# Kernel optimization log

Measured on AMD Instinct MI355X. Metric: run time of the kernel, lower is better.

## Reference

```python
import jax, jax.numpy as jnp
import numpy as np

N = 200000
B = 2
BEV_SIZES = [(376, 376), (188, 188), (94, 94), (188, 188), (94, 94)]
VOXELS = [40000, 20000, 10000, 20000, 10000]
IN_SCALES = 3
D_PT = 9        # point_feature_dim
D_AVFE = 64
D_AVFEO = 128
FINFO_MIN = float(np.finfo(np.float32).min)  # torch fills scatter_max output with finfo.min


def _make_vfs(V, H, W):
    # unique (batch, y, x) voxel coordinates for the dense scatter_nd
    total = B * H * W
    flat = np.arange(V, dtype=np.int64) * (total // V)
    b = flat // (H * W)
    r = flat % (H * W)
    return jnp.asarray(np.stack([b, r // W, r % W], axis=1), dtype=jnp.int32)


def setup_inputs():
    key = jax.random.key(0)
    ks = jax.random.split(key, 16)
    inp = {"points": jax.random.normal(ks[0], (N, 4), jnp.float32)}
    for i in range(5):
        inp[f"vlc{i}"] = jax.random.uniform(ks[1 + i], (N, 3), jnp.float32)
        inp[f"pv{i}"] = jax.random.randint(ks[6 + i], (N,), 0, VOXELS[i], dtype=jnp.int32)
        inp[f"vfs{i}"] = _make_vfs(VOXELS[i], *BEV_SIZES[i])
    s = 0.05
    inp["W_avfe_point"] = jax.random.normal(ks[11], (D_PT, D_AVFE), jnp.float32) * s
    inp["W_avfe_att"] = jax.random.normal(ks[12], (2 * D_PT, D_AVFE), jnp.float32) * s
    inp["W_avfeo_point"] = jax.random.normal(ks[13], (IN_SCALES * 2 * D_AVFE, D_AVFEO), jnp.float32) * s
    inp["W_avfeo_att"] = jax.random.normal(ks[14], (2 * D_PT, D_AVFEO), jnp.float32) * s
    inp["batch_size"] = B
    return inp


def _seg_mean_gather(x, idx, V):
    # scatterMean: per-voxel mean gathered back to points -> [N, C]
    s = jax.ops.segment_sum(x, idx, num_segments=V)
    cnt = jax.ops.segment_sum(jnp.ones((x.shape[0], 1), x.dtype), idx, num_segments=V)
    return (s / jnp.maximum(cnt, 1.0))[idx]


def _seg_max(x, idx, V):
    # scatterMax with torch finfo.min init for empty voxels
    return jnp.maximum(jax.ops.segment_max(x, idx, num_segments=V), FINFO_MIN)


def _scale_inputs(points, vlc, pv, V):
    pm = _seg_mean_gather(points, pv, V)                      # [N,4]
    plc = points[:, :3] - pm[:, :3]                            # [N,3]
    pif = jnp.concatenate([points, plc, vlc[:, :2]], axis=1)   # [N,9]
    a2 = _seg_mean_gather(pif, pv, V)                          # [N,9]
    a1 = jnp.concatenate([plc, pif[:, 3:]], axis=1)            # [N,9]
    att = jnp.concatenate([a1, a2], axis=1)                    # [N,18]
    return pif, att


def _dense(vfs, feat, batch_size, H, W):
    # scatter_nd into [B,H,W,C] then channels-first
    out = jnp.zeros((batch_size, H, W, feat.shape[1]), feat.dtype)
    out = out.at[vfs[:, 0], vfs[:, 1], vfs[:, 2]].set(feat)
    return jnp.transpose(out, (0, 3, 1, 2))


def reference(points, vlc0, vlc1, vlc2, vlc3, vlc4,
              W_avfe_point, W_avfe_att, W_avfeo_point, W_avfeo_att,
              pv0, pv1, pv2, pv3, pv4,
              vfs0, vfs1, vfs2, vfs3, vfs4, batch_size):
    vlcs = [vlc0, vlc1, vlc2, vlc3, vlc4]
    pvs = [pv0, pv1, pv2, pv3, pv4]
    vfss = [vfs0, vfs1, vfs2, vfs3, vfs4]

    avfe = []
    for i in range(IN_SCALES):
        V = vfss[i].shape[0]
        pif, att = _scale_inputs(points, vlcs[i], pvs[i], V)
        pfc = pif @ W_avfe_point                 # [N,64]
        afc = att @ W_avfe_att                   # [N,64]
        final = afc * pfc
        vf = _seg_max(final, pvs[i], V)          # [V,64]
        avfe.append(jnp.concatenate([final, vf[pvs[i]]], axis=1))  # [N,128]

    feat = jnp.concatenate(avfe, axis=1)         # [N,384]
    pfc_o = feat @ W_avfeo_point                 # [N,128]

    outs = []
    for i in range(IN_SCALES, len(vfss)):
        V = vfss[i].shape[0]
        pif, att = _scale_inputs(points, vlcs[i], pvs[i], V)
        afc = att @ W_avfeo_att                  # [N,128]
        final = afc * pfc_o
        vf = _seg_max(final, pvs[i], V)          # [V,128]
        H, W = BEV_SIZES[i]
        outs.append(_dense(vfss[i], vf, batch_size, H, W))
    return tuple(outs)
```

## Files before the change

### kernel.cpp

```cpp
#include <hip/hip_runtime.h>
#include <stdint.h>

#define N_PTS 200000
#define HW3 35344
#define HW4 8836
#define OUT4_OFF 9048064
#define OUT_ELEMS 11310080
#define S_FLOATS 1000000
#define F_UINTS  2240000
#define G_USHORTS 3840000
#define G4_OFF 2560000
typedef unsigned short ushort_t;

__device__ __forceinline__ float bfbits2f(unsigned hbits16) {
  return __uint_as_float(hbits16 << 16);
}
__device__ __forceinline__ ushort_t f2bf(float f) {
  if (!(f == f)) return (ushort_t)0;
  unsigned u = __float_as_uint(f);
  if ((u & 0x7F800000u) == 0x7F800000u)
    return (ushort_t)(((u >> 16) & 0x8000u) | 0x7F7Fu);
  unsigned r = u + 0x7FFFu + ((u >> 16) & 1u);
  ushort_t h = (ushort_t)(r >> 16);
  if ((h & 0x7FFFu) == 0x7F80u) h = (ushort_t)((h & 0x8000u) | 0x7F7Fu);
  return h;
}
__device__ __forceinline__ unsigned enc16(unsigned h) {
  return (h & 0x8000u) ? (h ^ 0xFFFFu) : (h | 0x8000u);
}
__device__ __forceinline__ unsigned dec16(unsigned e) {
  return (e & 0x8000u) ? (e & 0x7FFFu) : (e ^ 0xFFFFu);
}

__device__ __forceinline__ float decSafeF(unsigned e) {
  unsigned d = dec16(e & 0xFFFFu);
  if ((d & 0x7F80u) == 0x7F80u) d = 0;
  return bfbits2f(d);
}

__device__ __forceinline__ void casMax16(ushort_t* o16, size_t pos, unsigned enc) {
  unsigned* w = (unsigned*)(o16 + (pos & ~(size_t)1));
  unsigned sh = ((unsigned)pos & 1u) << 4;
  unsigned old = *w;
  while (true) {
    unsigned cur = (old >> sh) & 0xFFFFu;
    if (enc <= cur) break;
    unsigned nw = (old & ~(0xFFFFu << sh)) | (enc << sh);
    unsigned prev = atomicCAS(w, old, nw);
    if (prev == old) break;
    old = prev;
  }
}
__device__ __forceinline__ void casMaxPair(unsigned* w, unsigned lo, unsigned hi) {
  unsigned old = *w;
  while (true) {
    unsigned clo = old & 0xFFFFu, chi = old >> 16;
    unsigned nlo = lo > clo ? lo : clo;
    unsigned nhi = hi > chi ? hi : chi;
    unsigned nw = nlo | (nhi << 16);
    if (nw == old) break;
    unsigned prev = atomicCAS(w, old, nw);
    if (prev == old) break;
    old = prev;
  }
}

struct ScaleArgs {
  const ushort_t* vlc[5];
  const int*      pv[5];
  float*          stats[5];
  unsigned*       vf16[3];
};

__global__ void k_init(unsigned* __restrict__ outw, unsigned* __restrict__ g) {
  int i = blockIdx.x * blockDim.x + threadIdx.x;
  if (i < S_FLOATS) { outw[i] = 0u; return; }
  if (i < S_FLOATS + F_UINTS) { outw[i] = 0x00800080u; return; }
  i -= S_FLOATS + F_UINTS;
  if (i < G_USHORTS / 2) g[i] = 0x00800080u;
}

__global__ void __launch_bounds__(256) k_segsum(const ushort4* __restrict__ points, ScaleArgs a) {
  int p = blockIdx.x * blockDim.x + threadIdx.x;
  if (p >= N_PTS) return;
  ushort4 pu = points[p];
  float px = bfbits2f(pu.x), py = bfbits2f(pu.y), pz = bfbits2f(pu.z), pw = bfbits2f(pu.w);
  #pragma unroll
  for (int s = 0; s < 5; s++) {
    int v = a.pv[s][p];
    float l0 = bfbits2f(a.vlc[s][3 * p + 0]);
    float l1 = bfbits2f(a.vlc[s][3 * p + 1]);
    float* st = a.stats[s] + (size_t)v * 10;
    atomicAdd(st + 0, px);
    atomicAdd(st + 1, py);
    atomicAdd(st + 2, pz);
    atomicAdd(st + 3, pw);
    atomicAdd(st + 4, l0);
    atomicAdd(st + 5, l1);
    atomicAdd(st + 9, 1.0f);
  }
}

__global__ void k_voxstats(ScaleArgs a) {
  int i = blockIdx.x * blockDim.x + threadIdx.x;
  int s, v;
  if      (i <  40000) { s = 0; v = i; }
  else if (i <  60000) { s = 1; v = i - 40000; }
  else if (i <  70000) { s = 2; v = i - 60000; }
  else if (i <  90000) { s = 3; v = i - 70000; }
  else if (i < 100000) { s = 4; v = i - 90000; }
  else return;
  float* st = a.stats[s] + (size_t)v * 10;
  float cnt = st[9];
  float c = fmaxf(cnt, 1.0f);
  float s0 = st[0], s1 = st[1], s2 = st[2], s3 = st[3], s4 = st[4], s5 = st[5];
  float pm0 = s0 / c, pm1 = s1 / c, pm2 = s2 / c, pm3 = s3 / c;
  float mp0 = (s0 - cnt * pm0) / c;
  float mp1 = (s1 - cnt * pm1) / c;
  float mp2 = (s2 - cnt * pm2) / c;
  float mv0 = s4 / c, mv1 = s5 / c;
  st[0] = pm0; st[1] = pm1; st[2] = pm2; st[3] = pm3;
  st[4] = mp0; st[5] = mp1; st[6] = mp2; st[7] = mv0; st[8] = mv1;
}

__global__ void __launch_bounds__(256) k_scale012(
    const ushort4* __restrict__ points, ScaleArgs a,
    const ushort_t* __restrict__ Wp,
    const ushort_t* __restrict__ Wa) {
  __shared__ float WpS[9 * 64];
  __shared__ float WaS[18 * 64];
  int tid = threadIdx.x;
  for (int i = tid; i < 9 * 64; i += 256)  WpS[i] = bfbits2f(Wp[i]);
  for (int i = tid; i < 18 * 64; i += 256) WaS[i] = bfbits2f(Wa[i]);
  __syncthreads();

  int p = blockIdx.x * blockDim.x + tid;
  if (p >= N_PTS) return;
  ushort4 pu = points[p];
  float px = bfbits2f(pu.x), py = bfbits2f(pu.y), pz = bfbits2f(pu.z), pw = bfbits2f(pu.w);
  #pragma unroll 1
  for (int s = 0; s < 3; s++) {
    int v = a.pv[s][p];
    const float* st = a.stats[s] + (size_t)v * 10;
    float a2[9];
    #pragma unroll
    for (int k = 0; k < 9; k++) a2[k] = st[k];
    float plc0 = px - a2[0], plc1 = py - a2[1], plc2 = pz - a2[2];
    float vl0 = bfbits2f(a.vlc[s][3 * p + 0]);
    float vl1 = bfbits2f(a.vlc[s][3 * p + 1]);
    float pif[9] = {px, py, pz, pw, plc0, plc1, plc2, vl0, vl1};
    float att[18] = {plc0, plc1, plc2, pw, plc0, plc1, plc2, vl0, vl1,
                     a2[0], a2[1], a2[2], a2[3], a2[4], a2[5], a2[6], a2[7], a2[8]};
    unsigned* vfw = a.vf16[s] + (size_t)v * 32;
    #pragma unroll 1
    for (int cb = 0; cb < 64; cb += 16) {
      float accp[16], acca[16];
      #pragma unroll
      for (int l = 0; l < 16; l++) { accp[l] = 0.0f; acca[l] = 0.0f; }
      #pragma unroll
      for (int k = 0; k < 9; k++) {
        float x = pif[k];
        #pragma unroll
        for (int l = 0; l < 16; l++) accp[l] = fmaf(x, WpS[k * 64 + cb + l], accp[l]);
      }
      #pragma unroll
      for (int k = 0; k < 18; k++) {
        float x = att[k];
        #pragma unroll
        for (int l = 0; l < 16; l++) acca[l] = fmaf(x, WaS[k * 64 + cb + l], acca[l]);
      }
      #pragma unroll
      for (int l = 0; l < 16; l += 2) {
        unsigned lo = enc16(f2bf(acca[l] * accp[l]));
        unsigned hi = enc16(f2bf(acca[l + 1] * accp[l + 1]));
        casMaxPair(vfw + ((cb + l) >> 1), lo, hi);
      }
    }
  }
}

struct K4Args {
  const ushort4* points;
  const ushort_t* vlc[5];
  const int* pv[5];
  const float* stats[5];
  const unsigned* vf16[3];
  ushort_t* G;
  const ushort_t* Wp;
  const ushort_t* Wa;
  const ushort_t* Wpo;
  const ushort_t* Wao;
};

__global__ void __launch_bounds__(256, 2) k_big(K4Args a) {
  __shared__ __align__(16) float A[64][68];
  __shared__ __align__(16) unsigned Bw16[64][64];
  __shared__ __align__(16) float WaoS[18][128];
  __shared__ __align__(16) float WpS[9][64];
  __shared__ __align__(16) float WaS[18][64];
  __shared__ __align__(16) float attS[64][20];
  __shared__ int pvAll[5][64];

  int tid = threadIdx.x;
  int p0 = blockIdx.x * 64;

  for (int i = tid; i < 18 * 128; i += 256) WaoS[0][i] = bfbits2f(a.Wao[i]);
  for (int i = tid; i < 9 * 64; i += 256)   WpS[0][i]  = bfbits2f(a.Wp[i]);
  for (int i = tid; i < 18 * 64; i += 256)  WaS[0][i]  = bfbits2f(a.Wa[i]);
  if (tid < 64) {
    #pragma unroll
    for (int s = 0; s < 5; s++) pvAll[s][tid] = a.pv[s][p0 + tid];
  }
  float4 pt = make_float4(0.f, 0.f, 0.f, 0.f);
  if (tid < 64) {
    ushort4 pu = a.points[p0 + tid];
    pt = make_float4(bfbits2f(pu.x), bfbits2f(pu.y), bfbits2f(pu.z), bfbits2f(pu.w));
  }
  __syncthreads();

  int pr = tid & 7;
  int cg = tid >> 3;
  int cb4 = cg << 2;
  int cb2 = cg << 1;

  float acc[8][4];
  #pragma unroll
  for (int j = 0; j < 8; j++)
    #pragma unroll
    for (int l = 0; l < 4; l++) acc[j][l] = 0.0f;

  #pragma unroll 1
  for (int kc = 0; kc < 6; kc++) {
    {
      const uint4* src = (const uint4*)(a.Wpo + (size_t)kc * 64 * 128);
      uint4* dst = (uint4*)&Bw16[0][0];
      for (int i = tid; i < 1024; i += 256) dst[i] = src[i];
    }
    int s = kc >> 1;
    if ((kc & 1) == 0) {
      if (tid < 64) {
        int v = pvAll[s][tid];
        const float* st = a.stats[s] + (size_t)v * 10;
        float a2k[9];
        #pragma unroll
        for (int k = 0; k < 9; k++) a2k[k] = st[k];
        float vl0 = bfbits2f(a.vlc[s][3 * (p0 + tid) + 0]);
        float vl1 = bfbits2f(a.vlc[s][3 * (p0 + tid) + 1]);
        float* row = attS[tid];
        row[0] = pt.x; row[1] = pt.y; row[2] = pt.z; row[3] = pt.w;
        row[4] = pt.x - a2k[0]; row[5] = pt.y - a2k[1]; row[6] = pt.z - a2k[2];
        row[7] = vl0; row[8] = vl1;
        #pragma unroll
        for (int k = 0; k < 9; k++) row[9 + k] = a2k[k];
      }
      __syncthreads();
      int p = tid >> 2, ch0 = (tid & 3) << 4;
      float pv_[18];
      #pragma unroll
      for (int k = 0; k < 18; k++) pv_[k] = attS[p][k];
      float accp[16], acca[16];
      #pragma unroll
      for (int l = 0; l < 16; l++) { accp[l] = 0.0f; acca[l] = 0.0f; }
      #pragma unroll
      for (int k = 0; k < 9; k++) {
        float x = pv_[k];
        #pragma unroll
        for (int l = 0; l < 16; l++) accp[l] = fmaf(x, WpS[k][ch0 + l], accp[l]);
      }
      #pragma unroll
      for (int k = 0; k < 18; k++) {
        int src = (k < 3) ? (4 + k) : (k == 3) ? 3 : k;
        float x = pv_[src];
        #pragma unroll
        for (int l = 0; l < 16; l++) acca[l] = fmaf(x, WaS[k][ch0 + l], acca[l]);
      }
      #pragma unroll
      for (int l4 = 0; l4 < 16; l4 += 4) {
        float4 f;
        f.x = accp[l4 + 0] * acca[l4 + 0];
        f.y = accp[l4 + 1] * acca[l4 + 1];
        f.z = accp[l4 + 2] * acca[l4 + 2];
        f.w = accp[l4 + 3] * acca[l4 + 3];
        *(float4*)&A[p][ch0 + l4] = f;
      }
    } else {
      const unsigned* vfw = a.vf16[s];
      for (int i = tid; i < 2048; i += 256) {
        int p = i >> 5; int w = i & 31;
        int v = pvAll[s][p];
        unsigned q = vfw[(size_t)v * 32 + w];
        A[p][2 * w]     = decSafeF(q & 0xFFFFu);
        A[p][2 * w + 1] = decSafeF(q >> 16);
      }
    }
    __syncthreads();
    #pragma unroll 2
    for (int kk = 0; kk < 64; kk += 4) {
      float4 av[8];
      #pragma unroll
      for (int j = 0; j < 8; j++) av[j] = *(const float4*)&A[pr + (j << 3)][kk];
      #pragma unroll
      for (int t = 0; t < 4; t++) {
        unsigned w0 = Bw16[kk + t][cb2], w1 = Bw16[kk + t][cb2 + 1];
        float b0 = __uint_as_float(w0 << 16);
        float b1 = __uint_as_float(w0 & 0xFFFF0000u);
        float b2 = __uint_as_float(w1 << 16);
        float b3 = __uint_as_float(w1 & 0xFFFF0000u);
        #pragma unroll
        for (int j = 0; j < 8; j++) {
          float x = (t == 0) ? av[j].x : (t == 1) ? av[j].y : (t == 2) ? av[j].z : av[j].w;
          acc[j][0] = fmaf(x, b0, acc[j][0]);
          acc[j][1] = fmaf(x, b1, acc[j][1]);
          acc[j][2] = fmaf(x, b2, acc[j][2]);
          acc[j][3] = fmaf(x, b3, acc[j][3]);
        }
      }
    }
    __syncthreads();
  }

  #pragma unroll 1
  for (int si = 0; si < 2; si++) {
    if (tid < 64) {
      int v = pvAll[3 + si][tid];
      const float* st = a.stats[3 + si] + (size_t)v * 10;
      float a2k[9];
      #pragma unroll
      for (int k = 0; k < 9; k++) a2k[k] = st[k];
      float vl0 = bfbits2f(a.vlc[3 + si][3 * (p0 + tid) + 0]);
      float vl1 = bfbits2f(a.vlc[3 + si][3 * (p0 + tid) + 1]);
      float plc0 = pt.x - a2k[0], plc1 = pt.y - a2k[1], plc2 = pt.z - a2k[2];
      float* row = attS[tid];
      row[0] = plc0; row[1] = plc1; row[2] = plc2; row[3] = pt.w;
      row[4] = plc0; row[5] = plc1; row[6] = plc2; row[7] = vl0; row[8] = vl1;
      #pragma unroll
      for (int k = 0; k < 9; k++) row[9 + k] = a2k[k];
    }
    __syncthreads();
    size_t gbase = si ? (size_t)G4_OFF : 0;
    float afc[8][4];
    #pragma unroll
    for (int j = 0; j < 8; j++)
      #pragma unroll
      for (int l = 0; l < 4; l++) afc[j][l] = 0.0f;
    #pragma unroll
    for (int k = 0; k < 18; k++) {
      float4 w = *(const float4*)&WaoS[k][cb4];
      #pragma unroll
      for (int j = 0; j < 8; j++) {
        float x = attS[pr + (j << 3)][k];
        afc[j][0] = fmaf(x, w.x, afc[j][0]);
        afc[j][1] = fmaf(x, w.y, afc[j][1]);
        afc[j][2] = fmaf(x, w.z, afc[j][2]);
        afc[j][3] = fmaf(x, w.w, afc[j][3]);
      }
    }
    #pragma unroll
    for (int j = 0; j < 8; j++) {
      int p = pr + (j << 3);
      int v = pvAll[3 + si][p];
      #pragma unroll
      for (int l = 0; l < 4; l++) {
        float f = afc[j][l] * acc[j][l];
        casMax16(a.G, gbase + (size_t)v * 128 + (cb4 + l), enc16(f2bf(f)));
      }
    }
    __syncthreads();
  }
}

__global__ void k_clear(unsigned* __restrict__ outw) {
  int i = blockIdx.x * blockDim.x + threadIdx.x;
  if (i < OUT_ELEMS / 2) outw[i] = 0u;
}

__global__ void __launch_bounds__(256) k_scatter_out(const ushort_t* __restrict__ G,
                                                     const int* __restrict__ vfs3,
                                                     const int* __restrict__ vfs4,
                                                     ushort_t* __restrict__ out16) {
  int i = blockIdx.x * blockDim.x + threadIdx.x;
  if (i >= G_USHORTS) return;
  int s, idx;
  if (i < G4_OFF) { s = 0; idx = i; }
  else            { s = 1; idx = i - G4_OFF; }
  int v = idx >> 7, c = idx & 127;
  const int* vfs = s ? vfs4 : vfs3;
  int b = vfs[3 * v], y = vfs[3 * v + 1], x = vfs[3 * v + 2];
  size_t pos;
  if (s) pos = (size_t)OUT4_OFF + (((size_t)(b * 128 + c) * 94 + y) * 94 + x);
  else   pos = ((size_t)(b * 128 + c) * 188 + y) * 188 + x;
  unsigned d = dec16(G[i]);
  if ((d & 0x7F80u) == 0x7F80u) d = (d & 0x8000u) | 0x7F7Fu;
  out16[pos] = (ushort_t)d;
}

extern "C" void kernel_launch(void* const* d_in, const int* in_sizes, int n_in,
                              void* d_out, int out_size, void* d_ws, size_t ws_size,
                              hipStream_t stream) {
  static const int VOX[5] = {40000, 20000, 10000, 20000, 10000};

  const ushort_t* points = (const ushort_t*)d_in[0];
  const ushort_t* vlc[5]; const int* pv[5]; const int* vfs[5];
  const ushort_t *Wp, *Wa, *Wpo, *Wao;
  if (in_sizes[2] == N_PTS) {
    for (int s = 0; s < 5; s++) {
      vlc[s] = (const ushort_t*)d_in[1 + 3 * s];
      pv[s]  = (const int*)     d_in[2 + 3 * s];
      vfs[s] = (const int*)     d_in[3 + 3 * s];
    }
    Wp  = (const ushort_t*)d_in[16];
    Wa  = (const ushort_t*)d_in[17];
    Wpo = (const ushort_t*)d_in[18];
    Wao = (const ushort_t*)d_in[19];
  } else {
    for (int s = 0; s < 5; s++) vlc[s] = (const ushort_t*)d_in[1 + s];
    Wp  = (const ushort_t*)d_in[6];
    Wa  = (const ushort_t*)d_in[7];
    Wpo = (const ushort_t*)d_in[8];
    Wao = (const ushort_t*)d_in[9];
    for (int s = 0; s < 5; s++) pv[s]  = (const int*)d_in[10 + s];
    for (int s = 0; s < 5; s++) vfs[s] = (const int*)d_in[15 + s];
  }

  float* statsBase = (float*)d_out;
  unsigned* outw = (unsigned*)d_out;
  unsigned* fBase = outw + S_FLOATS;
  ushort_t* G = (ushort_t*)d_ws;
  ushort_t* out16 = (ushort_t*)d_out;

  float* stats[5];
  size_t offS = 0;
  for (int s = 0; s < 5; s++) { stats[s] = statsBase + offS; offS += (size_t)VOX[s] * 10; }
  unsigned* vf16[3];
  size_t offF = 0;
  for (int s = 0; s < 3; s++) { vf16[s] = fBase + offF; offF += (size_t)VOX[s] * 32; }

  ScaleArgs sa;
  for (int s = 0; s < 5; s++) { sa.vlc[s] = vlc[s]; sa.pv[s] = pv[s]; sa.stats[s] = stats[s]; }
  for (int s = 0; s < 3; s++) sa.vf16[s] = vf16[s];

  int totInit = S_FLOATS + F_UINTS + G_USHORTS / 2;
  k_init<<<(totInit + 255) / 256, 256, 0, stream>>>(outw, (unsigned*)d_ws);

  k_segsum<<<(N_PTS + 255) / 256, 256, 0, stream>>>((const ushort4*)points, sa);

  k_voxstats<<<(100000 + 255) / 256, 256, 0, stream>>>(sa);

  k_scale012<<<(N_PTS + 255) / 256, 256, 0, stream>>>((const ushort4*)points, sa, Wp, Wa);

  K4Args ka;
  ka.points = (const ushort4*)points;
  for (int s = 0; s < 5; s++) { ka.vlc[s] = vlc[s]; ka.pv[s] = pv[s]; ka.stats[s] = stats[s]; }
  for (int s = 0; s < 3; s++) ka.vf16[s] = vf16[s];
  ka.G = G;
  ka.Wp = Wp; ka.Wa = Wa; ka.Wpo = Wpo; ka.Wao = Wao;
  k_big<<<N_PTS / 64, 256, 0, stream>>>(ka);

  k_clear<<<(OUT_ELEMS / 2 + 255) / 256, 256, 0, stream>>>(outw);

  k_scatter_out<<<(G_USHORTS + 255) / 256, 256, 0, stream>>>(G, vfs[3], vfs[4], out16);
}
```

Before: 1.666 ms.

## Pair CAS max updates, reuse A smem for Wao, tile output scatter via LDS

The final segment-max in k_big now merges two adjacent bf16 channels per 32-bit CAS, which halves the number of atomic loops per point. The Wao weights are staged into the already-used A buffer instead of a dedicated shared array, lowering LDS use per block and possibly allowing more resident blocks. k_scatter_out is restructured to load a 32-voxel by 128-channel tile into shared memory, precompute the per-voxel output bases, and write channel-major so that each channel's stores come from one place. The decode of gathered max values also drops the NaN/Inf masking, which may change handling of empty-voxel sentinels.

After: 1.567 ms. 5.9% less time.

```diff
diff --git a/kernel.cpp b/kernel.cpp
--- a/kernel.cpp
+++ b/kernel.cpp
@@ -10,6 +10,8 @@
 #define F_UINTS  2240000
 #define G_USHORTS 3840000
 #define G4_OFF 2560000
+#define NB3 625
+#define NB4 313
 typedef unsigned short ushort_t;
 
 __device__ __forceinline__ float bfbits2f(unsigned hbits16) {
@@ -32,25 +34,6 @@
   return (e & 0x8000u) ? (e & 0x7FFFu) : (e ^ 0xFFFFu);
 }
 
-__device__ __forceinline__ float decSafeF(unsigned e) {
-  unsigned d = dec16(e & 0xFFFFu);
-  if ((d & 0x7F80u) == 0x7F80u) d = 0;
-  return bfbits2f(d);
-}
-
-__device__ __forceinline__ void casMax16(ushort_t* o16, size_t pos, unsigned enc) {
-  unsigned* w = (unsigned*)(o16 + (pos & ~(size_t)1));
-  unsigned sh = ((unsigned)pos & 1u) << 4;
-  unsigned old = *w;
-  while (true) {
-    unsigned cur = (old >> sh) & 0xFFFFu;
-    if (enc <= cur) break;
-    unsigned nw = (old & ~(0xFFFFu << sh)) | (enc << sh);
-    unsigned prev = atomicCAS(w, old, nw);
-    if (prev == old) break;
-    old = prev;
-  }
-}
 __device__ __forceinline__ void casMaxPair(unsigned* w, unsigned lo, unsigned hi) {
   unsigned old = *w;
   while (true) {
@@ -195,7 +178,6 @@
 __global__ void __launch_bounds__(256, 2) k_big(K4Args a) {
   __shared__ __align__(16) float A[64][68];
   __shared__ __align__(16) unsigned Bw16[64][64];
-  __shared__ __align__(16) float WaoS[18][128];
   __shared__ __align__(16) float WpS[9][64];
   __shared__ __align__(16) float WaS[18][64];
   __shared__ __align__(16) float attS[64][20];
@@ -204,7 +186,6 @@
   int tid = threadIdx.x;
   int p0 = blockIdx.x * 64;
 
-  for (int i = tid; i < 18 * 128; i += 256) WaoS[0][i] = bfbits2f(a.Wao[i]);
   for (int i = tid; i < 9 * 64; i += 256)   WpS[0][i]  = bfbits2f(a.Wp[i]);
   for (int i = tid; i < 18 * 64; i += 256)  WaS[0][i]  = bfbits2f(a.Wa[i]);
   if (tid < 64) {
@@ -286,11 +267,11 @@
     } else {
       const unsigned* vfw = a.vf16[s];
       for (int i = tid; i < 2048; i += 256) {
-        int p = i >> 5; int w = i & 31;
+        int p = i >> 5; int wd = i & 31;
         int v = pvAll[s][p];
-        unsigned q = vfw[(size_t)v * 32 + w];
-        A[p][2 * w]     = decSafeF(q & 0xFFFFu);
-        A[p][2 * w + 1] = decSafeF(q >> 16);
+        unsigned q = vfw[(size_t)v * 32 + wd];
+        A[p][2 * wd]     = bfbits2f(dec16(q & 0xFFFFu));
+        A[p][2 * wd + 1] = bfbits2f(dec16(q >> 16));
       }
     }
     __syncthreads();
@@ -319,6 +300,9 @@
     __syncthreads();
   }
 
+  float* WaoE = &A[0][0];
+  for (int i = tid; i < 18 * 128; i += 256) WaoE[i] = bfbits2f(a.Wao[i]);
+
   #pragma unroll 1
   for (int si = 0; si < 2; si++) {
     if (tid < 64) {
@@ -345,7 +329,7 @@
       for (int l = 0; l < 4; l++) afc[j][l] = 0.0f;
     #pragma unroll
     for (int k = 0; k < 18; k++) {
-      float4 w = *(const float4*)&WaoS[k][cb4];
+      float4 w = *(const float4*)&WaoE[k * 128 + cb4];
       #pragma unroll
       for (int j = 0; j < 8; j++) {
         float x = attS[pr + (j << 3)][k];
@@ -359,11 +343,13 @@
     for (int j = 0; j < 8; j++) {
       int p = pr + (j << 3);
       int v = pvAll[3 + si][p];
-      #pragma unroll
-      for (int l = 0; l < 4; l++) {
-        float f = afc[j][l] * acc[j][l];
-        casMax16(a.G, gbase + (size_t)v * 128 + (cb4 + l), enc16(f2bf(f)));
-      }
+      unsigned* gw = (unsigned*)a.G + ((gbase + (size_t)v * 128 + cb4) >> 1);
+      unsigned e0 = enc16(f2bf(afc[j][0] * acc[j][0]));
+      unsigned e1 = enc16(f2bf(afc[j][1] * acc[j][1]));
+      unsigned e2 = enc16(f2bf(afc[j][2] * acc[j][2]));
+      unsigned e3 = enc16(f2bf(afc[j][3] * acc[j][3]));
+      casMaxPair(gw, e0, e1);
+      casMaxPair(gw + 1, e2, e3);
     }
     __syncthreads();
   }
@@ -378,20 +364,40 @@
                                                      const int* __restrict__ vfs3,
                                                      const int* __restrict__ vfs4,
                                                      ushort_t* __restrict__ out16) {
-  int i = blockIdx.x * blockDim.x + threadIdx.x;
-  if (i >= G_USHORTS) return;
-  int s, idx;
-  if (i < G4_OFF) { s = 0; idx = i; }
-  else            { s = 1; idx = i - G4_OFF; }
-  int v = idx >> 7, c = idx & 127;
+  __shared__ ushort_t tile[32][130];
+  __shared__ int vbase[32];
+  int blk = blockIdx.x;
+  int s = (blk >= NB3) ? 1 : 0;
+  int v0 = (s ? (blk - NB3) : blk) * 32;
+  int V = s ? 10000 : 20000;
+  int HW = s ? HW4 : HW3;
+  int W = s ? 94 : 188;
   const int* vfs = s ? vfs4 : vfs3;
-  int b = vfs[3 * v], y = vfs[3 * v + 1], x = vfs[3 * v + 2];
-  size_t pos;
-  if (s) pos = (size_t)OUT4_OFF + (((size_t)(b * 128 + c) * 94 + y) * 94 + x);
-  else   pos = ((size_t)(b * 128 + c) * 188 + y) * 188 + x;
-  unsigned d = dec16(G[i]);
-  if ((d & 0x7F80u) == 0x7F80u) d = (d & 0x8000u) | 0x7F7Fu;
-  out16[pos] = (ushort_t)d;
+  size_t goff = s ? (size_t)G4_OFF : 0;
+  size_t ooff = s ? (size_t)OUT4_OFF : 0;
+  int nv = min(32, V - v0);
+  int tid = threadIdx.x;
+  const unsigned* gw = (const unsigned*)(G + goff);
+  for (int i = tid; i < nv * 64; i += 256) {
+    int vi = i >> 6, cw = i & 63;
+    unsigned q = gw[(size_t)(v0 + vi) * 64 + cw];
+    tile[vi][2 * cw]     = (ushort_t)(q & 0xFFFFu);
+    tile[vi][2 * cw + 1] = (ushort_t)(q >> 16);
+  }
+  if (tid < nv) {
+    int v = v0 + tid;
+    int b = vfs[3 * v], y = vfs[3 * v + 1], x = vfs[3 * v + 2];
+    vbase[tid] = (b * 128) * HW + y * W + x;
+  }
+  __syncthreads();
+  for (int i = tid; i < 128 * 32; i += 256) {
+    int c = i >> 5, vi = i & 31;
+    if (vi < nv) {
+      unsigned d = dec16(tile[vi][c]);
+      if ((d & 0x7F80u) == 0x7F80u) d = (d & 0x8000u) | 0x7F7Fu;
+      out16[ooff + (size_t)vbase[vi] + (size_t)c * HW] = (ushort_t)d;
+    }
+  }
 }
 
 extern "C" void kernel_launch(void* const* d_in, const int* in_sizes, int n_in,
@@ -458,5 +464,5 @@
 
   k_clear<<<(OUT_ELEMS / 2 + 255) / 256, 256, 0, stream>>>(outw);
 
-  k_scatter_out<<<(G_USHORTS + 255) / 256, 256, 0, stream>>>(G, vfs[3], vfs[4], out16);
-}
+  k_scatter_out<<<NB3 + NB4, 256, 0, stream>>>(G, vfs[3], vfs[4], out16);
+}
```
